# Performance work log

Measured on AMD Instinct MI355X. Metric: run time of the kernel, lower is better.

Reference implementation:

```python
import jax, jax.numpy as jnp
import numpy as np
from jax import lax

G, K, KS = 4, 16, 3            # stripes, latents per stripe, support kernel
TEMP, TOPK_RATIO, GATE, EPS = 0.125, 0.125, 0.05, 1e-6


def _l2norm(v):
    # F.normalize(p=2, dim=-1): divide by max(norm, 1e-12)
    return v / jnp.maximum(jnp.linalg.norm(v, axis=-1, keepdims=True), 1e-12)


def _avg_pool3(x):
    # 3x3 avg pool, stride 1, pad 1, count_include_pad=True (torch default)
    s = lax.reduce_window(x, 0.0, lax.add, (1, 1, KS, KS), (1, 1, 1, 1),
                          [(0, 0), (0, 0), (KS // 2, KS // 2), (KS // 2, KS // 2)])
    return s / float(KS * KS)


def setup_inputs() -> dict:
    key = jax.random.key(0)
    k1, k2 = jax.random.split(key)
    x = jax.random.normal(k1, (64, 256, 64, 44), dtype=jnp.float32)
    latent_basis = jax.random.normal(k2, (G, K, 256), dtype=jnp.float32) * 0.05
    return {"x": x, "latent_basis": latent_basis}


def reference(x, latent_basis):
    n, c, h, w = x.shape
    hs = h // G
    # 'n c (g hs) w -> (n g) c hs w'
    sf = x.reshape(n, c, G, hs, w).transpose(0, 2, 1, 3, 4).reshape(n * G, c, hs, w)
    support_feat = _avg_pool3(sf)
    feat_flat = sf.reshape(n, G, c, hs * w).transpose(0, 1, 3, 2)          # n g p c
    supp_flat = support_feat.reshape(n, G, c, hs * w).transpose(0, 1, 3, 2)  # n g p c
    # active mask from detached energy
    e = jnp.mean(lax.stop_gradient(sf) ** 2, axis=1)                       # [n*G, hs, w]
    e = e / jnp.maximum(jnp.max(e, axis=(-2, -1), keepdims=True), EPS)
    am = (e > GATE).astype(jnp.float32)
    fb = (e > 0).astype(jnp.float32)
    use_fb = jnp.sum(am, axis=(-2, -1), keepdims=True) <= 0
    am = jnp.where(use_fb, fb, am).reshape(n, G, hs * w)                   # n g p
    # routing
    sfn = _l2norm(supp_flat)
    lb = _l2norm(latent_basis)                                             # g k c
    logits = jnp.einsum('ngpc,gkc->ngpk', sfn, lb) / TEMP
    route = jax.nn.softmax(logits, axis=-1)
    supp = route * am[..., None]                                           # n g p k
    pw = supp / jnp.maximum(jnp.sum(supp, axis=2, keepdims=True), EPS)
    tokens = jnp.einsum('ngpk,ngpc->ngkc', pw, feat_flat)                  # n g k c
    tokens = tokens.transpose(0, 3, 1, 2).reshape(n, c, G * K)             # n c (g k)
    # presence via top-k over positions
    p = supp.shape[2]
    topk = max(1, min(p, int(p * TOPK_RATIO)))
    vals = lax.top_k(supp.transpose(0, 1, 3, 2), topk)[0]                  # n g k topk
    pres = jnp.mean(vals, axis=-1).reshape(n, G * K)
    pres = pres / jnp.maximum(jnp.sum(pres, axis=1, keepdims=True), EPS)
    return tokens, pres
```

## Files before the change

### kernel.cpp

```cpp
#include <hip/hip_runtime.h>
#include <cstdint>


#define C_ 256
#define W_ 44
#define P_ 704
#define CH_STRIDE 2816
#define NB_STRIDE 720896
#define TOPK_ 88
#define GATE_ 0.05f
#define EPS_ 1e-6f

#define DPP_WAVE_SHL1 0x130
#define DPP_WAVE_SHR1 0x138
__device__ __forceinline__ float dpp_from_left(float v) {
  return __int_as_float(__builtin_amdgcn_update_dpp(
      0, __float_as_int(v), DPP_WAVE_SHR1, 0xF, 0xF, true));
}
__device__ __forceinline__ float dpp_from_right(float v) {
  return __int_as_float(__builtin_amdgcn_update_dpp(
      0, __float_as_int(v), DPP_WAVE_SHL1, 0xF, 0xF, true));
}

__global__ __launch_bounds__(256) void k_norm_basis(const float* __restrict__ lb,
                                                    float* __restrict__ lbn) {
  int gk = blockIdx.x;
  int t = threadIdx.x;
  float v = lb[gk * 256 + t];
  float ss = v * v;
  #pragma unroll
  for (int off = 32; off >= 1; off >>= 1) ss += __shfl_xor(ss, off);
  __shared__ float red[4];
  if ((t & 63) == 0) red[t >> 6] = ss;
  __syncthreads();
  float tot = red[0] + red[1] + red[2] + red[3];
  float scale = 1.f / fmaxf(sqrtf(tot), 1e-12f);
  int g = gk >> 4, k = gk & 15;
  lbn[((g * 256 + t) << 4) + k] = v * scale;
}

#define LOAD_GRP(Pm, P0, Pp, cbase)                                    \
  { _Pragma("unroll")                                                  \
    for (int j_ = 0; j_ < 4; j_++) {                                   \
      const size_t o_ = (size_t)((cbase) + j_) * CH_STRIDE;            \
      Pm[j_] = xm[o_]; P0[j_] = xb[o_]; Pp[j_] = xp[o_];               \
    } }

#define CONS_GRP(Pm, P0, Pp, cbase)                                    \
  { _Pragma("unroll")                                                  \
    for (int j_ = 0; j_ < 4; j_++) {                                   \
      float a  = act ? P0[j_] : 0.f;                                   \
      float am_ = (act && hm) ? Pm[j_] : 0.f;                          \
      float ap_ = (act && hp) ? Pp[j_] : 0.f;                          \
      float vs = am_ + a + ap_;                                        \
      float lf = dpp_from_left(vs);                                    \
      float rt = dpp_from_right(vs);                                   \
      float win = lf + vs + rt;                                        \
      pw2 = fmaf(win, win, pw2);                                       \
      sq  = fmaf(a, a, sq);                                            \
      const int co_ = __builtin_amdgcn_readfirstlane(((cbase) + j_) << 4); \
      const float4* wp4 = (const float4*)(lbb + co_);                  \
      float4 w0 = wp4[0], w1 = wp4[1], w2 = wp4[2], w3 = wp4[3];       \
      rawdot[0]  = fmaf(a, w0.x, rawdot[0]);  rawdot[1]  = fmaf(a, w0.y, rawdot[1]);  \
      rawdot[2]  = fmaf(a, w0.z, rawdot[2]);  rawdot[3]  = fmaf(a, w0.w, rawdot[3]);  \
      rawdot[4]  = fmaf(a, w1.x, rawdot[4]);  rawdot[5]  = fmaf(a, w1.y, rawdot[5]);  \
      rawdot[6]  = fmaf(a, w1.z, rawdot[6]);  rawdot[7]  = fmaf(a, w1.w, rawdot[7]);  \
      rawdot[8]  = fmaf(a, w2.x, rawdot[8]);  rawdot[9]  = fmaf(a, w2.y, rawdot[9]);  \
      rawdot[10] = fmaf(a, w2.z, rawdot[10]); rawdot[11] = fmaf(a, w2.w, rawdot[11]); \
      rawdot[12] = fmaf(a, w3.x, rawdot[12]); rawdot[13] = fmaf(a, w3.y, rawdot[13]); \
      rawdot[14] = fmaf(a, w3.z, rawdot[14]); rawdot[15] = fmaf(a, w3.w, rawdot[15]); \
    } }

__global__ __launch_bounds__(1024, 4) void k_route(const float* __restrict__ x,
                                                   const float* __restrict__ lbn,
                                                   float* __restrict__ supp_pk,
                                                   float* __restrict__ invden_ws,
                                                   float* __restrict__ presraw) {
  __shared__ float rsl[11264];
  __shared__ uint32_t hist_l[16 * 256];
  __shared__ float redA[16];
  __shared__ float redB[16];
  __shared__ float redM[2];
  __shared__ float red2[16 * 16];

  const int tid = threadIdx.x;
  const int w = tid >> 6;
  const int l = tid & 63;
  const bool act = (l < 44);
  const int s = blockIdx.x, n = s >> 2, g = s & 3;
  const int p = w * 44 + l;

  const int lsafe = act ? l : 0;
  const float* xb = x + (size_t)n * NB_STRIDE + (g * 16 + w) * 44 + lsafe;
  const float* xm = xb + ((w > 0)  ? -44 : 0);
  const float* xp = xb + ((w < 15) ?  44 : 0);
  const bool hm = (w > 0), hp = (w < 15);

  const float* lbb = lbn + (g << 12);

  float rawdot[16];
  #pragma unroll
  for (int k = 0; k < 16; k++) rawdot[k] = 0.f;
  float sq = 0.f, pw2 = 0.f;

  float Avm[4], Av0[4], Avp[4];
  float Bvm[4], Bv0[4], Bvp[4];

  LOAD_GRP(Avm, Av0, Avp, 0)
  for (int c = 0; c < 256; c += 8) {
    LOAD_GRP(Bvm, Bv0, Bvp, c + 4)
    CONS_GRP(Avm, Av0, Avp, c)
    if (c + 8 < 256) { LOAD_GRP(Avm, Av0, Avp, c + 8) }
    CONS_GRP(Bvm, Bv0, Bvp, c + 4)
  }

  if (act) {
    #pragma unroll
    for (int k = 0; k < 16; k++) rsl[k * 704 + p] = rawdot[k];
  }
  __syncthreads();

  float pd[16];
  #pragma unroll
  for (int k = 0; k < 16; k++) pd[k] = 0.f;
  if (act) {
    #pragma unroll
    for (int dy = -1; dy <= 1; dy++) {
      int yy = w + dy;
      if (yy < 0 || yy > 15) continue;
      #pragma unroll
      for (int dx = -1; dx <= 1; dx++) {
        int xx = l + dx;
        if (xx < 0 || xx > 43) continue;
        int pp = yy * 44 + xx;
        #pragma unroll
        for (int k = 0; k < 16; k++) pd[k] += rsl[k * 704 + pp];
      }
    }
  }

  float e_raw = sq * (1.f / 256.f);
  float m = e_raw;
  #pragma unroll
  for (int off = 32; off >= 1; off >>= 1) m = fmaxf(m, __shfl_xor(m, off));
  if (l == 0) redA[w] = m;
  __syncthreads();
  if (tid == 0) {
    float mm = redA[0];
    for (int w2 = 1; w2 < 16; w2++) mm = fmaxf(mm, redA[w2]);
    redM[0] = mm;
  }
  __syncthreads();
  float M = fmaxf(redM[0], EPS_);
  float e = e_raw / M;
  float am = (e > GATE_) ? 1.f : 0.f;
  float fb = (e_raw > 0.f) ? 1.f : 0.f;
  float a = am;
  #pragma unroll
  for (int off = 32; off >= 1; off >>= 1) a += __shfl_xor(a, off);
  if (l == 0) redB[w] = a;
  __syncthreads();
  if (tid == 0) {
    float sm = 0.f;
    for (int w2 = 0; w2 < 16; w2++) sm += redB[w2];
    redM[1] = sm;
  }
  __syncthreads();
  if (redM[1] <= 0.f) am = fb;

  float pnorm = sqrtf(pw2) * (1.f / 9.f);
  float invn = 1.f / fmaxf(pnorm, 1e-12f);
  float scl = invn * (8.f / 9.f);
  float li[16];
  float mx = -1e30f;
  #pragma unroll
  for (int k = 0; k < 16; k++) { li[k] = pd[k] * scl; mx = fmaxf(mx, li[k]); }
  float ssum = 0.f;
  #pragma unroll
  for (int k = 0; k < 16; k++) { li[k] = __expf(li[k] - mx); ssum += li[k]; }
  float rs2 = am / ssum;
  float supp[16];
  #pragma unroll
  for (int k = 0; k < 16; k++) supp[k] = li[k] * rs2;

  if (act) {
    float* spk = supp_pk + ((size_t)s * 704 + p) * 16;
    #pragma unroll
    for (int kq = 0; kq < 4; kq++)
      ((float4*)spk)[kq] = make_float4(supp[kq*4+0], supp[kq*4+1],
                                       supp[kq*4+2], supp[kq*4+3]);
  }

  #pragma unroll
  for (int k = 0; k < 16; k++) {
    float v2 = act ? supp[k] : 0.f;
    #pragma unroll
    for (int off = 32; off >= 1; off >>= 1) v2 += __shfl_xor(v2, off);
    if (l == 0) red2[w * 16 + k] = v2;
  }
  __syncthreads();
  if (tid < 16) {
    float den = 0.f;
    for (int w2 = 0; w2 < 16; w2++) den += red2[w2 * 16 + tid];
    invden_ws[s * 16 + tid] = 1.f / fmaxf(den, EPS_);
  }

  if (act) {
    #pragma unroll
    for (int k = 0; k < 16; k++) rsl[k * 704 + p] = supp[k];
  }
  __syncthreads();

  {
    const int k = w;
    uint32_t key[11];
    #pragma unroll
    for (int j = 0; j < 11; j++)
      key[j] = __float_as_uint(rsl[k * 704 + l + 64 * j]);
    uint32_t* h = &hist_l[w * 256];
    uint32_t prefix = 0, remaining = TOPK_;
    #pragma unroll
    for (int b = 3; b >= 0; b--) {
      const int shift = b * 8;
      *(uint4*)&h[l * 4] = make_uint4(0u, 0u, 0u, 0u);
      uint32_t mhi = (b == 3) ? 0u : (0xFFFFFFFFu << (shift + 8));
      #pragma unroll
      for (int j = 0; j < 11; j++)
        if ((key[j] & mhi) == (prefix & mhi))
          atomicAdd(&h[(key[j] >> shift) & 255u], 1u);
      uint4 bn = *(uint4*)&h[l * 4];
      uint32_t T = bn.x + bn.y + bn.z + bn.w;
      uint32_t inc = T;
      #pragma unroll
      for (int off = 1; off < 64; off <<= 1) {
        uint32_t o = (uint32_t)__shfl_down((int)inc, off);
        if (l + off < 64) inc += o;
      }
      uint32_t excl = inc - T;
      uint32_t g3 = excl + bn.w, g2 = g3 + bn.z, g1 = g2 + bn.y, g0 = g1 + bn.x;
      uint32_t pk = 0u;
      if (g0 >= remaining && g1 < remaining) pk = ((uint32_t)(4*l+0) << 16) | (remaining - g1);
      if (g1 >= remaining && g2 < remaining) pk = ((uint32_t)(4*l+1) << 16) | (remaining - g2);
      if (g2 >= remaining && g3 < remaining) pk = ((uint32_t)(4*l+2) << 16) | (remaining - g3);
      if (g3 >= remaining && excl < remaining) pk = ((uint32_t)(4*l+3) << 16) | (remaining - excl);
      #pragma unroll
      for (int off = 32; off >= 1; off >>= 1) pk |= (uint32_t)__shfl_xor((int)pk, off);
      prefix |= ((pk >> 16) & 255u) << shift;
      remaining = pk & 0xFFFFu;
    }
    float tf = __uint_as_float(prefix);
    float sgt = 0.f; uint32_t cgt = 0u;
    #pragma unroll
    for (int j = 0; j < 11; j++)
      if (key[j] > prefix) { sgt += __uint_as_float(key[j]); cgt++; }
    #pragma unroll
    for (int off = 32; off >= 1; off >>= 1) {
      sgt += __shfl_xor(sgt, off);
      cgt += (uint32_t)__shfl_xor((int)cgt, off);
    }
    if (l == 0)
      presraw[s * 16 + k] = (sgt + (float)(TOPK_ - cgt) * tf) * (1.f / (float)TOPK_);
  }
}

__global__ __launch_bounds__(512, 4) void k_tokens(const float* __restrict__ x,
                                                   const float* __restrict__ supp_pk,
                                                   const float* __restrict__ invden,
                                                   float* __restrict__ out) {
  __shared__ float xl[4096];
  const int tid = threadIdx.x;
  const int bid = blockIdx.x;
  const int s = bid >> 1, chalf = bid & 1;
  const int n = s >> 2, g = s & 3;
  const int cl = tid & 127;
  const int q = tid >> 7;
  const int sblk = s * (704 * 16);

  const float* xs = x + (size_t)n * NB_STRIDE + (size_t)(chalf * 128) * CH_STRIDE + g * P_;

  const int li0 = tid, li1 = tid + 512;
  const int lc0 = li0 >> 3, lj0 = li0 & 7;
  const int lc1 = li1 >> 3, lj1 = li1 & 7;
  const float* gp0 = xs + (size_t)lc0 * CH_STRIDE + lj0 * 4;
  const float* gp1 = xs + (size_t)lc1 * CH_STRIDE + lj1 * 4;
  const int wo0 = lc0 * 32 + ((lj0 * 4) ^ ((lc0 & 7) * 4));
  const int wo1 = lc1 * 32 + ((lj1 * 4) ^ ((lc1 & 7) * 4));

  const int sw = (cl & 7) * 4;
  const int rbase = cl * 32;

  float acc[16];
  #pragma unroll
  for (int k = 0; k < 16; k++) acc[k] = 0.f;

  float4 r0 = *(const float4*)gp0;
  float4 r1 = *(const float4*)gp1;
  *(float4*)&xl[wo0] = r0;
  *(float4*)&xl[wo1] = r1;
  __syncthreads();

  for (int tt = 0; tt < 22; tt++) {
    const int p0 = tt * 32;
    float4 n0, n1;
    if (tt < 21) {
      n0 = *(const float4*)(gp0 + p0 + 32);
      n1 = *(const float4*)(gp1 + p0 + 32);
    }

    #pragma unroll
    for (int jj = 0; jj < 8; jj += 4) {
      const int pp0 = q * 8 + jj;
      float4 xv = *(const float4*)&xl[rbase + (pp0 ^ sw)];
      float xa[4] = {xv.x, xv.y, xv.z, xv.w};
      #pragma unroll
      for (int dj = 0; dj < 4; dj++) {
        int uofs = __builtin_amdgcn_readfirstlane(sblk + (p0 + pp0 + dj) * 16);
        const float4* sp = (const float4*)(supp_pk + uofs);
        float4 s0 = sp[0], s1 = sp[1], s2 = sp[2], s3 = sp[3];
        float a = xa[dj];
        acc[0]  += a * s0.x; acc[1]  += a * s0.y; acc[2]  += a * s0.z; acc[3]  += a * s0.w;
        acc[4]  += a * s1.x; acc[5]  += a * s1.y; acc[6]  += a * s1.z; acc[7]  += a * s1.w;
        acc[8]  += a * s2.x; acc[9]  += a * s2.y; acc[10] += a * s2.z; acc[11] += a * s2.w;
        acc[12] += a * s3.x; acc[13] += a * s3.y; acc[14] += a * s3.z; acc[15] += a * s3.w;
      }
    }

    __syncthreads();
    if (tt < 21) {
      *(float4*)&xl[wo0] = n0;
      *(float4*)&xl[wo1] = n1;
      __syncthreads();
    }
  }

  if (q >= 2) {
    float* dst = &xl[((q - 2) * 128 + cl) * 16];
    #pragma unroll
    for (int kq = 0; kq < 4; kq++)
      ((float4*)dst)[kq] = make_float4(acc[kq*4], acc[kq*4+1], acc[kq*4+2], acc[kq*4+3]);
  }
  __syncthreads();
  if (q < 2) {
    const float* src = &xl[(q * 128 + cl) * 16];
    #pragma unroll
    for (int k = 0; k < 16; k++) acc[k] += src[k];
  }
  __syncthreads();
  if (q == 1) {
    float* dst = &xl[cl * 16];
    #pragma unroll
    for (int kq = 0; kq < 4; kq++)
      ((float4*)dst)[kq] = make_float4(acc[kq*4], acc[kq*4+1], acc[kq*4+2], acc[kq*4+3]);
  }
  __syncthreads();
  if (q == 0) {
    const float* src = &xl[cl * 16];
    float* op = out + ((size_t)(n * 256 + chalf * 128 + cl) * 64) + g * 16;
    #pragma unroll
    for (int kq = 0; kq < 4; kq++) {
      int u = __builtin_amdgcn_readfirstlane(s * 16 + kq * 4);
      const float4 iv = *(const float4*)(invden + u);
      float4 o;
      o.x = (acc[kq*4+0] + src[kq*4+0]) * iv.x;
      o.y = (acc[kq*4+1] + src[kq*4+1]) * iv.y;
      o.z = (acc[kq*4+2] + src[kq*4+2]) * iv.z;
      o.w = (acc[kq*4+3] + src[kq*4+3]) * iv.w;
      ((float4*)op)[kq] = o;
    }
  }
}

__global__ __launch_bounds__(64) void k_pres(const float* __restrict__ presraw,
                                             float* __restrict__ out) {
  const int n = blockIdx.x, t = threadIdx.x;
  float v = presraw[n * 64 + t];
  float ssum = v;
  #pragma unroll
  for (int off = 32; off >= 1; off >>= 1) ssum += __shfl_xor(ssum, off);
  out[1048576 + n * 64 + t] = v / fmaxf(ssum, EPS_);
}

extern "C" void kernel_launch(void* const* d_in, const int* in_sizes, int n_in,
                              void* d_out, int out_size, void* d_ws, size_t ws_size,
                              hipStream_t stream) {
  (void)in_sizes; (void)n_in; (void)out_size; (void)ws_size;
  const float* x  = (const float*)d_in[0];
  const float* lb = (const float*)d_in[1];
  float* out = (float*)d_out;
  float* ws = (float*)d_ws;
  float* lbn_ws     = ws;
  float* invden_ws  = ws + 16384;
  float* presraw_ws = ws + 20480;
  float* supp_pk_ws = ws + 2908160;

  k_norm_basis<<<64, 256, 0, stream>>>(lb, lbn_ws);
  k_route<<<256, 1024, 0, stream>>>(x, lbn_ws, supp_pk_ws, invden_ws, presraw_ws);
  k_tokens<<<512, 512, 0, stream>>>(x, supp_pk_ws, invden_ws, out);
  k_pres<<<64, 64, 0, stream>>>(presraw_ws, out);
}
```

Baseline: 333.1 us.

## Fuse token aggregation into routing kernel, keeping supp weights in LDS

Drops the separate k_tokens kernel and computes the weighted token sums inside k_route. The supp weights stay in shared memory instead of round-tripping through a global workspace, and invden is kept in LDS. x is re-read from global per block in 16-position tiles with two barriers per tile. The cost is higher LDS use per block, launch bounds lowered to one block per SM, and a serialized 44-step loop over all 256 channels within only 256 blocks, which may lower parallelism compared with the 512-block token kernel.

```diff
diff --git a/kernel.cpp b/kernel.cpp
--- a/kernel.cpp
+++ b/kernel.cpp
@@ -71,17 +71,20 @@
       rawdot[14] = fmaf(a, w3.z, rawdot[14]); rawdot[15] = fmaf(a, w3.w, rawdot[15]); \
     } }
 
-__global__ __launch_bounds__(1024, 4) void k_route(const float* __restrict__ x,
+__global__ __launch_bounds__(1024, 1) void k_route(const float* __restrict__ x,
                                                    const float* __restrict__ lbn,
-                                                   float* __restrict__ supp_pk,
-                                                   float* __restrict__ invden_ws,
+                                                   float* __restrict__ out,
                                                    float* __restrict__ presraw) {
   __shared__ float rsl[11264];
-  __shared__ uint32_t hist_l[16 * 256];
+  __shared__ float sl2[11264];
+  __shared__ uint32_t scratch16[4096];
   __shared__ float redA[16];
   __shared__ float redB[16];
   __shared__ float redM[2];
   __shared__ float red2[16 * 16];
+  __shared__ float invden_l[16];
+
+  float* xl2f = (float*)scratch16;
 
   const int tid = threadIdx.x;
   const int w = tid >> 6;
@@ -184,7 +187,9 @@
   for (int k = 0; k < 16; k++) supp[k] = li[k] * rs2;
 
   if (act) {
-    float* spk = supp_pk + ((size_t)s * 704 + p) * 16;
+    #pragma unroll
+    for (int k = 0; k < 16; k++) rsl[k * 704 + p] = supp[k];
+    float* spk = &sl2[p * 16];
     #pragma unroll
     for (int kq = 0; kq < 4; kq++)
       ((float4*)spk)[kq] = make_float4(supp[kq*4+0], supp[kq*4+1],
@@ -202,16 +207,86 @@
   if (tid < 16) {
     float den = 0.f;
     for (int w2 = 0; w2 < 16; w2++) den += red2[w2 * 16 + tid];
-    invden_ws[s * 16 + tid] = 1.f / fmaxf(den, EPS_);
-  }
-
-  if (act) {
-    #pragma unroll
-    for (int k = 0; k < 16; k++) rsl[k * 704 + p] = supp[k];
+    invden_l[tid] = 1.f / fmaxf(den, EPS_);
   }
   __syncthreads();
 
   {
+    const int sc = tid >> 2;
+    const int sj = tid & 3;
+    const float* gps = x + (size_t)n * NB_STRIDE + (size_t)sc * CH_STRIDE
+                         + g * 704 + sj * 4;
+    const int wos = sc * 16 + ((sj ^ (sc & 3)) << 2);
+    const int cl2 = tid & 255;
+    const int q2 = tid >> 8;
+    const int rdo = cl2 * 16 + (((q2 ^ (cl2 & 3))) << 2);
+
+    float acc2[16];
+    #pragma unroll
+    for (int k = 0; k < 16; k++) acc2[k] = 0.f;
+
+    for (int tt = 0; tt < 44; tt++) {
+      float4 r = *(const float4*)(gps + tt * 16);
+      __syncthreads();
+      *(float4*)&xl2f[wos] = r;
+      __syncthreads();
+      float4 xv = *(const float4*)&xl2f[rdo];
+      float xa[4] = {xv.x, xv.y, xv.z, xv.w};
+      const int pbase = (tt * 16 + q2 * 4) * 16;
+      #pragma unroll
+      for (int dj = 0; dj < 4; dj++) {
+        const float4* sp = (const float4*)&sl2[pbase + dj * 16];
+        float4 s0 = sp[0], s1 = sp[1], s2 = sp[2], s3 = sp[3];
+        float av = xa[dj];
+        acc2[0]  += av * s0.x; acc2[1]  += av * s0.y; acc2[2]  += av * s0.z; acc2[3]  += av * s0.w;
+        acc2[4]  += av * s1.x; acc2[5]  += av * s1.y; acc2[6]  += av * s1.z; acc2[7]  += av * s1.w;
+        acc2[8]  += av * s2.x; acc2[9]  += av * s2.y; acc2[10] += av * s2.z; acc2[11] += av * s2.w;
+        acc2[12] += av * s3.x; acc2[13] += av * s3.y; acc2[14] += av * s3.z; acc2[15] += av * s3.w;
+      }
+    }
+    __syncthreads();
+
+    if (q2 >= 2) {
+      float* dst = &sl2[((q2 - 2) * 256 + cl2) * 16];
+      #pragma unroll
+      for (int kq = 0; kq < 4; kq++)
+        ((float4*)dst)[kq] = make_float4(acc2[kq*4], acc2[kq*4+1],
+                                         acc2[kq*4+2], acc2[kq*4+3]);
+    }
+    __syncthreads();
+    if (q2 < 2) {
+      const float* src = &sl2[(q2 * 256 + cl2) * 16];
+      #pragma unroll
+      for (int k = 0; k < 16; k++) acc2[k] += src[k];
+    }
+    __syncthreads();
+    if (q2 == 1) {
+      float* dst = &sl2[cl2 * 16];
+      #pragma unroll
+      for (int kq = 0; kq < 4; kq++)
+        ((float4*)dst)[kq] = make_float4(acc2[kq*4], acc2[kq*4+1],
+                                         acc2[kq*4+2], acc2[kq*4+3]);
+    }
+    __syncthreads();
+    if (q2 == 0) {
+      const float* src = &sl2[cl2 * 16];
+      float* op = out + ((size_t)(n * 256 + cl2) * 64) + g * 16;
+      #pragma unroll
+      for (int kq = 0; kq < 4; kq++) {
+        const float4 iv = *(const float4*)&invden_l[kq * 4];
+        float4 o;
+        o.x = (acc2[kq*4+0] + src[kq*4+0]) * iv.x;
+        o.y = (acc2[kq*4+1] + src[kq*4+1]) * iv.y;
+        o.z = (acc2[kq*4+2] + src[kq*4+2]) * iv.z;
+        o.w = (acc2[kq*4+3] + src[kq*4+3]) * iv.w;
+        ((float4*)op)[kq] = o;
+      }
+    }
+  }
+  __syncthreads();
+
+  {
+    uint32_t* hist_l = scratch16;
     const int k = w;
     uint32_t key[11];
     #pragma unroll
@@ -263,113 +338,6 @@
   }
 }
 
-__global__ __launch_bounds__(512, 4) void k_tokens(const float* __restrict__ x,
-                                                   const float* __restrict__ supp_pk,
-                                                   const float* __restrict__ invden,
-                                                   float* __restrict__ out) {
-  __shared__ float xl[4096];
-  const int tid = threadIdx.x;
-  const int bid = blockIdx.x;
-  const int s = bid >> 1, chalf = bid & 1;
-  const int n = s >> 2, g = s & 3;
-  const int cl = tid & 127;
-  const int q = tid >> 7;
-  const int sblk = s * (704 * 16);
-
-  const float* xs = x + (size_t)n * NB_STRIDE + (size_t)(chalf * 128) * CH_STRIDE + g * P_;
-
-  const int li0 = tid, li1 = tid + 512;
-  const int lc0 = li0 >> 3, lj0 = li0 & 7;
-  const int lc1 = li1 >> 3, lj1 = li1 & 7;
-  const float* gp0 = xs + (size_t)lc0 * CH_STRIDE + lj0 * 4;
-  const float* gp1 = xs + (size_t)lc1 * CH_STRIDE + lj1 * 4;
-  const int wo0 = lc0 * 32 + ((lj0 * 4) ^ ((lc0 & 7) * 4));
-  const int wo1 = lc1 * 32 + ((lj1 * 4) ^ ((lc1 & 7) * 4));
-
-  const int sw = (cl & 7) * 4;
-  const int rbase = cl * 32;
-
-  float acc[16];
-  #pragma unroll
-  for (int k = 0; k < 16; k++) acc[k] = 0.f;
-
-  float4 r0 = *(const float4*)gp0;
-  float4 r1 = *(const float4*)gp1;
-  *(float4*)&xl[wo0] = r0;
-  *(float4*)&xl[wo1] = r1;
-  __syncthreads();
-
-  for (int tt = 0; tt < 22; tt++) {
-    const int p0 = tt * 32;
-    float4 n0, n1;
-    if (tt < 21) {
-      n0 = *(const float4*)(gp0 + p0 + 32);
-      n1 = *(const float4*)(gp1 + p0 + 32);
-    }
-
-    #pragma unroll
-    for (int jj = 0; jj < 8; jj += 4) {
-      const int pp0 = q * 8 + jj;
-      float4 xv = *(const float4*)&xl[rbase + (pp0 ^ sw)];
-      float xa[4] = {xv.x, xv.y, xv.z, xv.w};
-      #pragma unroll
-      for (int dj = 0; dj < 4; dj++) {
-        int uofs = __builtin_amdgcn_readfirstlane(sblk + (p0 + pp0 + dj) * 16);
-        const float4* sp = (const float4*)(supp_pk + uofs);
-        float4 s0 = sp[0], s1 = sp[1], s2 = sp[2], s3 = sp[3];
-        float a = xa[dj];
-        acc[0]  += a * s0.x; acc[1]  += a * s0.y; acc[2]  += a * s0.z; acc[3]  += a * s0.w;
-        acc[4]  += a * s1.x; acc[5]  += a * s1.y; acc[6]  += a * s1.z; acc[7]  += a * s1.w;
-        acc[8]  += a * s2.x; acc[9]  += a * s2.y; acc[10] += a * s2.z; acc[11] += a * s2.w;
-        acc[12] += a * s3.x; acc[13] += a * s3.y; acc[14] += a * s3.z; acc[15] += a * s3.w;
-      }
-    }
-
-    __syncthreads();
-    if (tt < 21) {
-      *(float4*)&xl[wo0] = n0;
-      *(float4*)&xl[wo1] = n1;
-      __syncthreads();
-    }
-  }
-
-  if (q >= 2) {
-    float* dst = &xl[((q - 2) * 128 + cl) * 16];
-    #pragma unroll
-    for (int kq = 0; kq < 4; kq++)
-      ((float4*)dst)[kq] = make_float4(acc[kq*4], acc[kq*4+1], acc[kq*4+2], acc[kq*4+3]);
-  }
-  __syncthreads();
-  if (q < 2) {
-    const float* src = &xl[(q * 128 + cl) * 16];
-    #pragma unroll
-    for (int k = 0; k < 16; k++) acc[k] += src[k];
-  }
-  __syncthreads();
-  if (q == 1) {
-    float* dst = &xl[cl * 16];
-    #pragma unroll
-    for (int kq = 0; kq < 4; kq++)
-      ((float4*)dst)[kq] = make_float4(acc[kq*4], acc[kq*4+1], acc[kq*4+2], acc[kq*4+3]);
-  }
-  __syncthreads();
-  if (q == 0) {
-    const float* src = &xl[cl * 16];
-    float* op = out + ((size_t)(n * 256 + chalf * 128 + cl) * 64) + g * 16;
-    #pragma unroll
-    for (int kq = 0; kq < 4; kq++) {
-      int u = __builtin_amdgcn_readfirstlane(s * 16 + kq * 4);
-      const float4 iv = *(const float4*)(invden + u);
-      float4 o;
-      o.x = (acc[kq*4+0] + src[kq*4+0]) * iv.x;
-      o.y = (acc[kq*4+1] + src[kq*4+1]) * iv.y;
-      o.z = (acc[kq*4+2] + src[kq*4+2]) * iv.z;
-      o.w = (acc[kq*4+3] + src[kq*4+3]) * iv.w;
-      ((float4*)op)[kq] = o;
-    }
-  }
-}
-
 __global__ __launch_bounds__(64) void k_pres(const float* __restrict__ presraw,
                                              float* __restrict__ out) {
   const int n = blockIdx.x, t = threadIdx.x;
@@ -389,12 +357,9 @@
   float* out = (float*)d_out;
   float* ws = (float*)d_ws;
   float* lbn_ws     = ws;
-  float* invden_ws  = ws + 16384;
   float* presraw_ws = ws + 20480;
-  float* supp_pk_ws = ws + 2908160;
 
   k_norm_basis<<<64, 256, 0, stream>>>(lb, lbn_ws);
-  k_route<<<256, 1024, 0, stream>>>(x, lbn_ws, supp_pk_ws, invden_ws, presraw_ws);
-  k_tokens<<<512, 512, 0, stream>>>(x, supp_pk_ws, invden_ws, out);
+  k_route<<<256, 1024, 0, stream>>>(x, lbn_ws, out, presraw_ws);
   k_pres<<<64, 64, 0, stream>>>(presraw_ws, out);
 }
```

Result: no change. 331.2 us (-0.6%).
